# Optimization experiments

Measured on AMD Instinct MI355X. Metric: run time of the kernel, lower is better.

## Reference

```python
import jax, jax.numpy as jnp
import numpy as np

B, T, E = 4, 2048, 512
H, D = 8, 64            # num_heads, head_size = E // H
HID = H * E             # FFN hidden = num_heads * n_embed (per source)
EPS = 1e-5


def layer_norm(x, g, b):
    mu = jnp.mean(x, axis=-1, keepdims=True)
    var = jnp.var(x, axis=-1, keepdims=True)
    return (x - mu) * jax.lax.rsqrt(var + EPS) * g + b


def setup_inputs() -> dict:
    key = jax.random.key(0)
    ks = jax.random.split(key, 12)
    s_e = 1.0 / np.sqrt(E)
    s_hd = 1.0 / np.sqrt(H * D)
    s_hid = 1.0 / np.sqrt(HID)
    return {
        "x": jax.random.normal(ks[0], (B, T, E), jnp.float32),
        "Wq": jax.random.normal(ks[1], (H, E, D), jnp.float32) * s_e,
        "Wk": jax.random.normal(ks[2], (H, E, D), jnp.float32) * s_e,
        "Wv": jax.random.normal(ks[3], (H, E, D), jnp.float32) * s_e,
        "Wo": jax.random.normal(ks[4], (H * D, E), jnp.float32) * s_hd,
        "bo": jnp.zeros((E,), jnp.float32),
        "W1": jax.random.normal(ks[5], (E, HID), jnp.float32) * s_e,
        "b1": jnp.zeros((HID,), jnp.float32),
        "W2": jax.random.normal(ks[6], (HID, E), jnp.float32) * s_hid,
        "b2": jnp.zeros((E,), jnp.float32),
        "g1": jnp.ones((E,), jnp.float32),
        "be1": jnp.zeros((E,), jnp.float32),
        "g2": jnp.ones((E,), jnp.float32),
        "be2": jnp.zeros((E,), jnp.float32),
    }


def reference(x, Wq, Wk, Wv, Wo, bo, W1, b1, W2, b2, g1, be1, g2, be2):
    # pre-LN decoder block (layer_norm_first=True path)
    xn = layer_norm(x, g1, be1)

    # multi-head causal attention; NOTE: scale is T**-0.5 per the source code
    q = jnp.einsum('bte,hed->bhtd', xn, Wq)
    k = jnp.einsum('bte,hed->bhtd', xn, Wk)
    v = jnp.einsum('bte,hed->bhtd', xn, Wv)
    scores = jnp.einsum('bhtd,bhsd->bhts', q, k) * (T ** -0.5)
    causal = jnp.tril(jnp.ones((T, T), bool))
    scores = jnp.where(causal, scores, -jnp.inf)
    attn = jax.nn.softmax(scores, axis=-1)
    o = jnp.einsum('bhts,bhsd->bhtd', attn, v)           # [B,H,T,D]
    o = o.transpose(0, 2, 1, 3).reshape(B, T, H * D)      # concat heads
    mha = o @ Wo + bo

    x = xn + mha
    xn2 = layer_norm(x, g2, be2)
    ffn = jax.nn.relu(xn2 @ W1 + b1) @ W2 + b2
    return xn2 + ffn
```

## Files before the change

kernel.cpp:

```cpp
#include <hip/hip_runtime.h>
#include <hip/hip_bf16.h>
#include <math.h>

#define Bsz 4
#define Tt 2048
#define Ee 512
#define Hh 8
#define Dd 64
#define HIDs 4096
#define Mrows (Bsz * Tt)

typedef __attribute__((ext_vector_type(8))) short short8;
typedef __attribute__((ext_vector_type(4))) float f32x4;

#define AS1 __attribute__((address_space(1)))
#define AS3 __attribute__((address_space(3)))

__device__ __forceinline__ unsigned short f2bfu(float f) {
    unsigned u = __float_as_uint(f);
    return (unsigned short)((u + 0x7fffu + ((u >> 16) & 1u)) >> 16);
}
__device__ __forceinline__ unsigned short truncbf(float f) {
    return (unsigned short)(__float_as_uint(f) >> 16);
}
__device__ __forceinline__ unsigned scale2(unsigned w, float s) {
    float lo = __uint_as_float(w << 16) * s;
    float hi = __uint_as_float(w & 0xffff0000u) * s;
    return (unsigned)f2bfu(lo) | ((unsigned)f2bfu(hi) << 16);
}

__global__ __launch_bounds__(256) void ln_kernel(const float* __restrict__ x,
        const float* __restrict__ g, const float* __restrict__ b,
        const float* __restrict__ addb,
        float* __restrict__ out_f, __hip_bfloat16* __restrict__ out_bf) {
    int row = blockIdx.x;
    int tid = threadIdx.x;
    const float* xr = x + (size_t)row * Ee;
    float v0 = xr[tid];
    float v1 = xr[tid + 256];
    float s = v0 + v1;
    float sq = v0 * v0 + v1 * v1;
#pragma unroll
    for (int off = 32; off > 0; off >>= 1) {
        s  += __shfl_xor(s, off, 64);
        sq += __shfl_xor(sq, off, 64);
    }
    __shared__ float ls[4], lq[4];
    int wid = tid >> 6, lane = tid & 63;
    if (lane == 0) { ls[wid] = s; lq[wid] = sq; }
    __syncthreads();
    s  = ls[0] + ls[1] + ls[2] + ls[3];
    sq = lq[0] + lq[1] + lq[2] + lq[3];
    float mean = s * (1.0f / Ee);
    float var  = sq * (1.0f / Ee) - mean * mean;
    float rstd = rsqrtf(var + 1e-5f);
    float o0 = (v0 - mean) * rstd * g[tid]       + b[tid];
    float o1 = (v1 - mean) * rstd * g[tid + 256] + b[tid + 256];
    float* orow = out_f + (size_t)row * Ee;
    orow[tid]       = o0 + addb[tid];
    orow[tid + 256] = o1 + addb[tid + 256];
    __hip_bfloat16* brow = out_bf + (size_t)row * Ee;
    brow[tid]       = __float2bfloat16(o0);
    brow[tid + 256] = __float2bfloat16(o1);
}

__device__ __forceinline__ void tr_tile(const float* __restrict__ in,
        __hip_bfloat16* __restrict__ outp, int R, int C, int c0, int r0) {
    __shared__ float tile[64][65];
    int tc = threadIdx.x & 63, tg = threadIdx.x >> 6;
#pragma unroll
    for (int i = 0; i < 16; ++i) {
        int r = tg * 16 + i;
        tile[r][tc] = in[(size_t)(r0 + r) * C + c0 + tc];
    }
    __syncthreads();
#pragma unroll
    for (int i = 0; i < 16; ++i) {
        int cc = tg * 16 + i;
        outp[(size_t)(c0 + cc) * R + r0 + tc] = __float2bfloat16(tile[tc][cc]);
    }
}
__global__ __launch_bounds__(256) void repack_all(const float* __restrict__ Wq,
        const float* __restrict__ Wk, const float* __restrict__ Wv,
        const float* __restrict__ Wo, const float* __restrict__ W1,
        const float* __restrict__ W2, __hip_bfloat16* __restrict__ bqT,
        __hip_bfloat16* __restrict__ woT, __hip_bfloat16* __restrict__ w1T,
        __hip_bfloat16* __restrict__ w2T) {
    int blk = blockIdx.x;
    if (blk < 192) {
        int p = blk >> 6, h = (blk >> 3) & 7, et = blk & 7;
        const float* W = (p == 0) ? Wq : ((p == 1) ? Wk : Wv);
        __shared__ float tile[64][65];
        int td = threadIdx.x & 63, tg = threadIdx.x >> 6;
#pragma unroll
        for (int i = 0; i < 16; ++i) {
            int e = tg * 16 + i;
            tile[e][td] = W[((size_t)h * Ee + et * 64 + e) * Dd + td];
        }
        __syncthreads();
#pragma unroll
        for (int i = 0; i < 16; ++i) {
            int d = tg * 16 + i;
            bqT[((size_t)(p * 512 + h * 64 + d)) * Ee + et * 64 + td] =
                __float2bfloat16(tile[td][d]);
        }
    } else if (blk < 256) {
        int t = blk - 192;
        tr_tile(Wo, woT, 512, 512, (t & 7) * 64, (t >> 3) * 64);
    } else if (blk < 768) {
        int t = blk - 256;
        tr_tile(W1, w1T, 512, HIDs, (t & 63) * 64, (t >> 6) * 64);
    } else {
        int t = blk - 768;
        tr_tile(W2, w2T, HIDs, 512, (t & 7) * 64, (t >> 3) * 64);
    }
}

__global__ __launch_bounds__(256) void mfma_gemm(
        const __hip_bfloat16* __restrict__ A, int lda,
        const __hip_bfloat16* __restrict__ B, int ldb,
        __hip_bfloat16* __restrict__ Cb, int ldc, int K, int nx) {
    __shared__ __hip_bfloat16 As[2 * 128 * 32];
    __shared__ __hip_bfloat16 Bs[2 * 128 * 32];
    int tid = threadIdx.x;
    int lane = tid & 63, wave = tid >> 6;
    int wm = wave >> 1, wn = wave & 1;
    int L = blockIdx.x;
    int slots = (int)gridDim.x >> 3;
    int v = (L & 7) * slots + (L >> 3);
    int bx = v % nx, by = v / nx;
    int row0 = by * 128, col0 = bx * 128;
    f32x4 acc[4][4];
#pragma unroll
    for (int i = 0; i < 4; ++i)
#pragma unroll
        for (int j = 0; j < 4; ++j) acc[i][j] = (f32x4){0.f, 0.f, 0.f, 0.f};

    int fr = lane & 15;
    int kq = (lane >> 4) << 3;

    for (int k0 = 0; k0 < K; k0 += 64) {
        __syncthreads();
#pragma unroll
        for (int j = 0; j < 4; ++j) {
            int c  = j * 256 + tid;
            int cb = j * 256 + wave * 64;
            int p  = c >> 9, cp = c & 511;
            int r  = cp >> 2, kg = (cp & 3) << 3;
            int ko = k0 + p * 32 + kg;
            __builtin_amdgcn_global_load_lds(
                (const AS1 void*)(A + (size_t)(row0 + r) * lda + ko),
                (AS3 void*)(As + cb * 8), 16, 0, 0);
            __builtin_amdgcn_global_load_lds(
                (const AS1 void*)(B + (size_t)(col0 + r) * ldb + ko),
                (AS3 void*)(Bs + cb * 8), 16, 0, 0);
        }
        __syncthreads();
#pragma unroll
        for (int ks = 0; ks < 2; ++ks) {
            short8 afr[4], bfr[4];
#pragma unroll
            for (int i = 0; i < 4; ++i) {
                afr[i] = *(const short8*)(As + ks * 4096 + (wm * 64 + i * 16 + fr) * 32 + kq);
                bfr[i] = *(const short8*)(Bs + ks * 4096 + (wn * 64 + i * 16 + fr) * 32 + kq);
            }
#pragma unroll
            for (int i = 0; i < 4; ++i)
#pragma unroll
                for (int j = 0; j < 4; ++j)
                    acc[i][j] = __builtin_amdgcn_mfma_f32_16x16x32_bf16(afr[i], bfr[j], acc[i][j], 0, 0, 0);
        }
    }
    int rq = (lane >> 4) << 2;
#pragma unroll
    for (int i = 0; i < 4; ++i)
#pragma unroll
        for (int j = 0; j < 4; ++j)
#pragma unroll
            for (int gidx = 0; gidx < 4; ++gidx) {
                int r = row0 + wm * 64 + i * 16 + rq + gidx;
                int c = col0 + wn * 64 + j * 16 + fr;
                Cb[(size_t)r * ldc + c] = __float2bfloat16(acc[i][j][gidx]);
            }
}

__global__ __launch_bounds__(256) void mfma_gemm_n64(
        const __hip_bfloat16* __restrict__ A, int lda,
        const __hip_bfloat16* __restrict__ B, int ldb,
        float* __restrict__ Cf, int ldc, int K, int nx) {
    __shared__ __hip_bfloat16 As[2 * 128 * 32];
    __shared__ __hip_bfloat16 Bs[2 * 64 * 32];
    int tid = threadIdx.x;
    int lane = tid & 63, wave = tid >> 6;
    int L = blockIdx.x;
    int slots = (int)gridDim.x >> 3;
    int v = (L & 7) * slots + (L >> 3);
    int bx = v % nx, by = v / nx;
    int row0 = by * 128, col0 = bx * 64;
    f32x4 acc[2][4];
#pragma unroll
    for (int i = 0; i < 2; ++i)
#pragma unroll
        for (int j = 0; j < 4; ++j) acc[i][j] = (f32x4){0.f, 0.f, 0.f, 0.f};

    int fr = lane & 15;
    int kq = (lane >> 4) << 3;

    for (int k0 = 0; k0 < K; k0 += 64) {
        __syncthreads();
#pragma unroll
        for (int j = 0; j < 4; ++j) {
            int c  = j * 256 + tid;
            int cb = j * 256 + wave * 64;
            int p  = c >> 9, cp = c & 511;
            int r  = cp >> 2, kg = (cp & 3) << 3;
            __builtin_amdgcn_global_load_lds(
                (const AS1 void*)(A + (size_t)(row0 + r) * lda + k0 + p * 32 + kg),
                (AS3 void*)(As + cb * 8), 16, 0, 0);
        }
#pragma unroll
        for (int j = 0; j < 2; ++j) {
            int c  = j * 256 + tid;
            int cb = j * 256 + wave * 64;
            int p  = c >> 8, cp = c & 255;
            int r  = cp >> 2, kg = (cp & 3) << 3;
            __builtin_amdgcn_global_load_lds(
                (const AS1 void*)(B + (size_t)(col0 + r) * ldb + k0 + p * 32 + kg),
                (AS3 void*)(Bs + cb * 8), 16, 0, 0);
        }
        __syncthreads();
#pragma unroll
        for (int ks = 0; ks < 2; ++ks) {
            short8 afr[2], bfr[4];
#pragma unroll
            for (int i = 0; i < 2; ++i)
                afr[i] = *(const short8*)(As + ks * 4096 + (wave * 32 + i * 16 + fr) * 32 + kq);
#pragma unroll
            for (int j = 0; j < 4; ++j)
                bfr[j] = *(const short8*)(Bs + ks * 2048 + (j * 16 + fr) * 32 + kq);
#pragma unroll
            for (int i = 0; i < 2; ++i)
#pragma unroll
                for (int j = 0; j < 4; ++j)
                    acc[i][j] = __builtin_amdgcn_mfma_f32_16x16x32_bf16(afr[i], bfr[j], acc[i][j], 0, 0, 0);
        }
    }
    int rq = (lane >> 4) << 2;
#pragma unroll
    for (int i = 0; i < 2; ++i)
#pragma unroll
        for (int j = 0; j < 4; ++j)
#pragma unroll
            for (int gidx = 0; gidx < 4; ++gidx) {
                int r = row0 + wave * 32 + i * 16 + rq + gidx;
                int c = col0 + j * 16 + fr;
                Cf[(size_t)r * ldc + c] += acc[i][j][gidx];
            }
}

__global__ __launch_bounds__(256) void mfma_gemm256(
        const __hip_bfloat16* __restrict__ A, int lda,
        const __hip_bfloat16* __restrict__ B, int ldb,
        __hip_bfloat16* __restrict__ Cb, int ldc, int K,
        const float* __restrict__ bias) {
    __shared__ __hip_bfloat16 As[2 * 256 * 32];
    __shared__ __hip_bfloat16 Bs[2 * 128 * 32];
    int tid = threadIdx.x;
    int lane = tid & 63, wave = tid >> 6;
    int L = blockIdx.x;
    int k8 = L & 7, sub = L >> 3;
    int sr = k8 >> 1, sc = k8 & 1;
    int by = sr * 8 + (sub >> 4);
    int bx = sc * 16 + (sub & 15);
    int row0 = by * 256, col0 = bx * 128;
    f32x4 acc[4][8];
#pragma unroll
    for (int i = 0; i < 4; ++i)
#pragma unroll
        for (int j = 0; j < 8; ++j) acc[i][j] = (f32x4){0.f, 0.f, 0.f, 0.f};

    int fr = lane & 15;
    int kq = (lane >> 4) << 3;

    for (int k0 = 0; k0 < K; k0 += 64) {
        __syncthreads();
#pragma unroll
        for (int j = 0; j < 8; ++j) {
            int c  = j * 256 + tid;
            int cb = j * 256 + wave * 64;
            int p  = c >> 10, cp = c & 1023;
            int r  = cp >> 2, kg = (cp & 3) << 3;
            __builtin_amdgcn_global_load_lds(
                (const AS1 void*)(A + (size_t)(row0 + r) * lda + k0 + p * 32 + kg),
                (AS3 void*)(As + cb * 8), 16, 0, 0);
        }
#pragma unroll
        for (int j = 0; j < 4; ++j) {
            int c  = j * 256 + tid;
            int cb = j * 256 + wave * 64;
            int p  = c >> 9, cp = c & 511;
            int r  = cp >> 2, kg = (cp & 3) << 3;
            __builtin_amdgcn_global_load_lds(
                (const AS1 void*)(B + (size_t)(col0 + r) * ldb + k0 + p * 32 + kg),
                (AS3 void*)(Bs + cb * 8), 16, 0, 0);
        }
        __syncthreads();
#pragma unroll
        for (int ks = 0; ks < 2; ++ks) {
            short8 afr[4], bfr[8];
#pragma unroll
            for (int i = 0; i < 4; ++i)
                afr[i] = *(const short8*)(As + ks * 8192 + (wave * 64 + i * 16 + fr) * 32 + kq);
#pragma unroll
            for (int j = 0; j < 8; ++j)
                bfr[j] = *(const short8*)(Bs + ks * 4096 + (j * 16 + fr) * 32 + kq);
#pragma unroll
            for (int i = 0; i < 4; ++i)
#pragma unroll
                for (int j = 0; j < 8; ++j)
                    acc[i][j] = __builtin_amdgcn_mfma_f32_16x16x32_bf16(afr[i], bfr[j], acc[i][j], 0, 0, 0);
        }
    }
    int rq = (lane >> 4) << 2;
    float bv[8];
#pragma unroll
    for (int j = 0; j < 8; ++j) bv[j] = bias[col0 + j * 16 + fr];
#pragma unroll
    for (int i = 0; i < 4; ++i)
#pragma unroll
        for (int j = 0; j < 8; ++j)
#pragma unroll
            for (int gidx = 0; gidx < 4; ++gidx) {
                int r = row0 + wave * 64 + i * 16 + rq + gidx;
                int c = col0 + j * 16 + fr;
                float t = acc[i][j][gidx] + bv[j];
                Cb[(size_t)r * ldc + c] = __float2bfloat16(t > 0.f ? t : 0.f);
            }
}

__global__ __launch_bounds__(512) void attn_mfma(const __hip_bfloat16* __restrict__ qkvb,
        __hip_bfloat16* __restrict__ ob) {
    __shared__ __hip_bfloat16 KsS[64 * 72];
    __shared__ __hip_bfloat16 VtS[64 * 72];
    __shared__ __hip_bfloat16 PsS[8 * 16 * 72];
    __hip_bfloat16* Qs = PsS;

    const unsigned short* q16 = (const unsigned short*)qkvb;
    int tid  = threadIdx.x;
    int lane = tid & 63, wave = tid >> 6;
    int g = lane >> 4, c = lane & 15;
    int blk = blockIdx.x;
    int qb  = 15 - (blk >> 5);
    int bh  = blk & 31;
    int b = bh >> 3, h = bh & 7;
    int base = qb * 128;
    size_t tokbase = (size_t)b * Tt;
    int qoff = h * 64, koff = 512 + h * 64, voff = 1024 + h * 64;
    const float qscale = 0.022097086912079608f * 1.4426950408889634f;

    {
        int q = tid >> 2, dg = (tid & 3) * 16;
        const unsigned short* src = q16 + (tokbase + base + q) * 1536 + qoff + dg;
        uint4 a  = *(const uint4*)src;
        uint4 b4 = *(const uint4*)(src + 8);
        uint4 ra, rb;
        ra.x = scale2(a.x, qscale);  ra.y = scale2(a.y, qscale);
        ra.z = scale2(a.z, qscale);  ra.w = scale2(a.w, qscale);
        rb.x = scale2(b4.x, qscale); rb.y = scale2(b4.y, qscale);
        rb.z = scale2(b4.z, qscale); rb.w = scale2(b4.w, qscale);
        *(uint4*)(Qs + q * 72 + dg)     = ra;
        *(uint4*)(Qs + q * 72 + dg + 8) = rb;
    }
    __syncthreads();
    short8 aq[2];
    aq[0] = *(const short8*)(Qs + (wave * 16 + c) * 72 + g * 8);
    aq[1] = *(const short8*)(Qs + (wave * 16 + c) * 72 + 32 + g * 8);

    short8 ones;
#pragma unroll
    for (int i = 0; i < 8; ++i) ones[i] = (short)0x3F80;

    f32x4 acc[4];
#pragma unroll
    for (int dt = 0; dt < 4; ++dt) acc[dt] = (f32x4){0.f, 0.f, 0.f, 0.f};
    f32x4 accL = (f32x4){0.f, 0.f, 0.f, 0.f};
    __hip_bfloat16* Psw = PsS + wave * (16 * 72);
    unsigned short* Psw16 = (unsigned short*)Psw;

    int tmax = 2 * qb + 1;
    for (int tile = 0; tile <= tmax; ++tile) {
        int s0 = tile * 64;
        __syncthreads();
        {
            int s = tid >> 3, dg = (tid & 7) * 8;
            *(uint4*)(KsS + s * 72 + dg) =
                *(const uint4*)(q16 + (tokbase + s0 + s) * 1536 + koff + dg);
        }
        {
            int sp = (tid & 31) * 2, dg4 = (tid >> 5) * 4;
            const unsigned short* r0p = q16 + (tokbase + s0 + sp) * 1536 + voff + dg4;
            uint2 va = *(const uint2*)r0p;
            uint2 vb = *(const uint2*)(r0p + 1536);
            unsigned a0[2] = {va.x, va.y};
            unsigned b0[2] = {vb.x, vb.y};
#pragma unroll
            for (int i = 0; i < 2; ++i) {
                unsigned p0 = (a0[i] & 0xffffu) | (b0[i] << 16);
                unsigned p1 = (a0[i] >> 16) | (b0[i] & 0xffff0000u);
                *(unsigned*)(VtS + (dg4 + 2 * i) * 72 + sp)     = p0;
                *(unsigned*)(VtS + (dg4 + 2 * i + 1) * 72 + sp) = p1;
            }
        }
        __syncthreads();
        if (tile == tmax && wave < 4) continue;
        f32x4 Sc[4];
#pragma unroll
        for (int st = 0; st < 4; ++st) Sc[st] = (f32x4){0.f, 0.f, 0.f, 0.f};
#pragma unroll
        for (int ks = 0; ks < 2; ++ks)
#pragma unroll
            for (int st = 0; st < 4; ++st) {
                short8 bk = *(const short8*)(KsS + (st * 16 + c) * 72 + ks * 32 + g * 8);
                Sc[st] = __builtin_amdgcn_mfma_f32_16x16x32_bf16(aq[ks], bk, Sc[st], 0, 0, 0);
            }
        if (tile >= 2 * qb) {
            int qg = base + wave * 16 + g * 4;
#pragma unroll
            for (int st = 0; st < 4; ++st) {
                int sg = s0 + st * 16 + c;
#pragma unroll
                for (int r = 0; r < 4; ++r)
                    if (sg > qg + r) Sc[st][r] = -1e30f;
            }
        }
#pragma unroll
        for (int st = 0; st < 4; ++st)
#pragma unroll
            for (int r = 0; r < 4; ++r)
                Psw16[(g * 4 + r) * 72 + st * 16 + c] =
                    truncbf(__builtin_amdgcn_exp2f(Sc[st][r]));
#pragma unroll
        for (int ks = 0; ks < 2; ++ks) {
            short8 ap = *(const short8*)(Psw + c * 72 + ks * 32 + g * 8);
            accL = __builtin_amdgcn_mfma_f32_16x16x32_bf16(ap, ones, accL, 0, 0, 0);
#pragma unroll
            for (int dt = 0; dt < 4; ++dt) {
                short8 bv = *(const short8*)(VtS + (dt * 16 + c) * 72 + ks * 32 + g * 8);
                acc[dt] = __builtin_amdgcn_mfma_f32_16x16x32_bf16(ap, bv, acc[dt], 0, 0, 0);
            }
        }
    }
    float rl[4];
#pragma unroll
    for (int r = 0; r < 4; ++r) rl[r] = 1.0f / accL[r];
#pragma unroll
    for (int dt = 0; dt < 4; ++dt)
#pragma unroll
        for (int r = 0; r < 4; ++r) {
            int row = base + wave * 16 + g * 4 + r;
            float o = acc[dt][r] * rl[r];
            ob[(tokbase + row) * 512 + h * 64 + dt * 16 + c] = __float2bfloat16(o);
        }
}

extern "C" void kernel_launch(void* const* d_in, const int* in_sizes, int n_in,
                              void* d_out, int out_size, void* d_ws, size_t ws_size,
                              hipStream_t stream) {
    const float* x   = (const float*)d_in[0];
    const float* Wq  = (const float*)d_in[1];
    const float* Wk  = (const float*)d_in[2];
    const float* Wv  = (const float*)d_in[3];
    const float* Wo  = (const float*)d_in[4];
    const float* bo  = (const float*)d_in[5];
    const float* W1  = (const float*)d_in[6];
    const float* b1  = (const float*)d_in[7];
    const float* W2  = (const float*)d_in[8];
    const float* b2  = (const float*)d_in[9];
    const float* g1  = (const float*)d_in[10];
    const float* be1 = (const float*)d_in[11];
    const float* g2  = (const float*)d_in[12];
    const float* be2 = (const float*)d_in[13];
    float* out = (float*)d_out;

    char* ws = (char*)d_ws;
    __hip_bfloat16* bqT    = (__hip_bfloat16*)(ws);
    __hip_bfloat16* woT    = (__hip_bfloat16*)(ws + 1572864);
    __hip_bfloat16* w1T    = (__hip_bfloat16*)(ws + 2097152);
    __hip_bfloat16* w2T    = (__hip_bfloat16*)(ws + 6291456);
    float*          xn     = (float*)(ws + 10485760);
    __hip_bfloat16* xn_bf  = (__hip_bfloat16*)(ws + 27262976);
    __hip_bfloat16* qkv_bf = (__hip_bfloat16*)(ws + 35651584);
    __hip_bfloat16* o_bf   = (__hip_bfloat16*)(ws + 60817408);
    __hip_bfloat16* h_bf   = (__hip_bfloat16*)(ws + 35651584);

    ln_kernel<<<Mrows, 256, 0, stream>>>(x, g1, be1, bo, xn, xn_bf);
    repack_all<<<1280, 256, 0, stream>>>(Wq, Wk, Wv, Wo, W1, W2, bqT, woT, w1T, w2T);
    mfma_gemm<<<768, 256, 0, stream>>>(
        xn_bf, 512, bqT, 512, qkv_bf, 1536, 512, 12);
    attn_mfma<<<Bsz * Hh * (Tt / 128), 512, 0, stream>>>(qkv_bf, o_bf);
    mfma_gemm_n64<<<512, 256, 0, stream>>>(
        o_bf, 512, woT, 512, xn, 512, 512, 8);
    ln_kernel<<<Mrows, 256, 0, stream>>>(xn, g2, be2, b2, out, xn_bf);
    mfma_gemm256<<<1024, 256, 0, stream>>>(
        xn_bf, 512, w1T, 512, h_bf, HIDs, 512, b1);
    mfma_gemm_n64<<<512, 256, 0, stream>>>(
        h_bf, HIDs, w2T, HIDs, out, 512, HIDs, 8);
}
```

Measured before the change: 355.2 us.

## Fold Q scale into weights, double-buffer GEMM, prefetch K/V in attention

The softmax scale and log2e factor move into the Wq repack, so the attention kernel no longer rescales Q tiles at load. The FFN-style GEMM drops from a 64-wide K step with two syncs to a 32-wide double-buffered LDS pipeline that issues the next stage's loads before the current MFMAs. The attention kernel prefetches the next K/V tile into registers while computing on the current one. Together these aim to hide global-load latency and remove per-tile ALU work. The cost is more register pressure, and Q is now rounded to bf16 once after scaling instead of being rescaled in the kernel.

Measured after the change: 342.3 us. -3.6%, faster.

```diff
diff --git a/kernel.cpp b/kernel.cpp
--- a/kernel.cpp
+++ b/kernel.cpp
@@ -22,11 +22,6 @@
 }
 __device__ __forceinline__ unsigned short truncbf(float f) {
     return (unsigned short)(__float_as_uint(f) >> 16);
-}
-__device__ __forceinline__ unsigned scale2(unsigned w, float s) {
-    float lo = __uint_as_float(w << 16) * s;
-    float hi = __uint_as_float(w & 0xffff0000u) * s;
-    return (unsigned)f2bfu(lo) | ((unsigned)f2bfu(hi) << 16);
 }
 
 __global__ __launch_bounds__(256) void ln_kernel(const float* __restrict__ x,
@@ -90,12 +85,13 @@
     if (blk < 192) {
         int p = blk >> 6, h = (blk >> 3) & 7, et = blk & 7;
         const float* W = (p == 0) ? Wq : ((p == 1) ? Wk : Wv);
+        float sc = (p == 0) ? 0.022097086912079608f * 1.4426950408889634f : 1.0f;
         __shared__ float tile[64][65];
         int td = threadIdx.x & 63, tg = threadIdx.x >> 6;
 #pragma unroll
         for (int i = 0; i < 16; ++i) {
             int e = tg * 16 + i;
-            tile[e][td] = W[((size_t)h * Ee + et * 64 + e) * Dd + td];
+            tile[e][td] = W[((size_t)h * Ee + et * 64 + e) * Dd + td] * sc;
         }
         __syncthreads();
 #pragma unroll
@@ -281,46 +277,52 @@
 
     int fr = lane & 15;
     int kq = (lane >> 4) << 3;
-
-    for (int k0 = 0; k0 < K; k0 += 64) {
-        __syncthreads();
-#pragma unroll
-        for (int j = 0; j < 8; ++j) {
-            int c  = j * 256 + tid;
-            int cb = j * 256 + wave * 64;
-            int p  = c >> 10, cp = c & 1023;
-            int r  = cp >> 2, kg = (cp & 3) << 3;
-            __builtin_amdgcn_global_load_lds(
-                (const AS1 void*)(A + (size_t)(row0 + r) * lda + k0 + p * 32 + kg),
-                (AS3 void*)(As + cb * 8), 16, 0, 0);
-        }
-#pragma unroll
-        for (int j = 0; j < 4; ++j) {
-            int c  = j * 256 + tid;
-            int cb = j * 256 + wave * 64;
-            int p  = c >> 9, cp = c & 511;
-            int r  = cp >> 2, kg = (cp & 3) << 3;
-            __builtin_amdgcn_global_load_lds(
-                (const AS1 void*)(B + (size_t)(col0 + r) * ldb + k0 + p * 32 + kg),
-                (AS3 void*)(Bs + cb * 8), 16, 0, 0);
-        }
-        __syncthreads();
-#pragma unroll
-        for (int ks = 0; ks < 2; ++ks) {
-            short8 afr[4], bfr[8];
-#pragma unroll
-            for (int i = 0; i < 4; ++i)
-                afr[i] = *(const short8*)(As + ks * 8192 + (wave * 64 + i * 16 + fr) * 32 + kq);
+    int nsteps = K >> 5;
+
+#define STAGE256(st, buf)                                                     \
+    do {                                                                      \
+        int ko_ = (st) << 5;                                                  \
+        _Pragma("unroll")                                                     \
+        for (int j = 0; j < 4; ++j) {                                         \
+            int c = j * 256 + tid;                                            \
+            int cb = j * 256 + wave * 64;                                     \
+            int r = c >> 2, kg = (c & 3) << 3;                                \
+            __builtin_amdgcn_global_load_lds(                                 \
+                (const AS1 void*)(A + (size_t)(row0 + r) * lda + ko_ + kg),   \
+                (AS3 void*)(As + (buf) * 8192 + cb * 8), 16, 0, 0);           \
+        }                                                                     \
+        _Pragma("unroll")                                                     \
+        for (int j = 0; j < 2; ++j) {                                         \
+            int c = j * 256 + tid;                                            \
+            int cb = j * 256 + wave * 64;                                     \
+            int r = c >> 2, kg = (c & 3) << 3;                                \
+            __builtin_amdgcn_global_load_lds(                                 \
+                (const AS1 void*)(B + (size_t)(col0 + r) * ldb + ko_ + kg),   \
+                (AS3 void*)(Bs + (buf) * 4096 + cb * 8), 16, 0, 0);           \
+        }                                                                     \
+    } while (0)
+
+    STAGE256(0, 0);
+    __syncthreads();
+    for (int st = 0; st < nsteps; ++st) {
+        int buf = st & 1;
+        if (st + 1 < nsteps) STAGE256(st + 1, buf ^ 1);
+        short8 afr[4], bfr[8];
+#pragma unroll
+        for (int i = 0; i < 4; ++i)
+            afr[i] = *(const short8*)(As + buf * 8192 + (wave * 64 + i * 16 + fr) * 32 + kq);
+#pragma unroll
+        for (int j = 0; j < 8; ++j)
+            bfr[j] = *(const short8*)(Bs + buf * 4096 + (j * 16 + fr) * 32 + kq);
+#pragma unroll
+        for (int i = 0; i < 4; ++i)
 #pragma unroll
             for (int j = 0; j < 8; ++j)
-                bfr[j] = *(const short8*)(Bs + ks * 4096 + (j * 16 + fr) * 32 + kq);
-#pragma unroll
-            for (int i = 0; i < 4; ++i)
-#pragma unroll
-                for (int j = 0; j < 8; ++j)
-                    acc[i][j] = __builtin_amdgcn_mfma_f32_16x16x32_bf16(afr[i], bfr[j], acc[i][j], 0, 0, 0);
-        }
-    }
+                acc[i][j] = __builtin_amdgcn_mfma_f32_16x16x32_bf16(afr[i], bfr[j], acc[i][j], 0, 0, 0);
+        __syncthreads();
+    }
+#undef STAGE256
+
     int rq = (lane >> 4) << 2;
     float bv[8];
 #pragma unroll
@@ -356,20 +358,14 @@
     int base = qb * 128;
     size_t tokbase = (size_t)b * Tt;
     int qoff = h * 64, koff = 512 + h * 64, voff = 1024 + h * 64;
-    const float qscale = 0.022097086912079608f * 1.4426950408889634f;
 
     {
         int q = tid >> 2, dg = (tid & 3) * 16;
         const unsigned short* src = q16 + (tokbase + base + q) * 1536 + qoff + dg;
         uint4 a  = *(const uint4*)src;
         uint4 b4 = *(const uint4*)(src + 8);
-        uint4 ra, rb;
-        ra.x = scale2(a.x, qscale);  ra.y = scale2(a.y, qscale);
-        ra.z = scale2(a.z, qscale);  ra.w = scale2(a.w, qscale);
-        rb.x = scale2(b4.x, qscale); rb.y = scale2(b4.y, qscale);
-        rb.z = scale2(b4.z, qscale); rb.w = scale2(b4.w, qscale);
-        *(uint4*)(Qs + q * 72 + dg)     = ra;
-        *(uint4*)(Qs + q * 72 + dg + 8) = rb;
+        *(uint4*)(Qs + q * 72 + dg)     = a;
+        *(uint4*)(Qs + q * 72 + dg + 8) = b4;
     }
     __syncthreads();
     short8 aq[2];
@@ -387,20 +383,21 @@
     __hip_bfloat16* Psw = PsS + wave * (16 * 72);
     unsigned short* Psw16 = (unsigned short*)Psw;
 
+    int s_k = tid >> 3, dg_k = (tid & 7) * 8;
+    int sp = (tid & 31) * 2, dg4 = (tid >> 5) * 4;
+    uint4 kreg; uint2 va, vb;
+    {
+        kreg = *(const uint4*)(q16 + (tokbase + s_k) * 1536 + koff + dg_k);
+        const unsigned short* r0p = q16 + (tokbase + sp) * 1536 + voff + dg4;
+        va = *(const uint2*)r0p;
+        vb = *(const uint2*)(r0p + 1536);
+    }
+
     int tmax = 2 * qb + 1;
     for (int tile = 0; tile <= tmax; ++tile) {
-        int s0 = tile * 64;
-        __syncthreads();
+        __syncthreads();
+        *(uint4*)(KsS + s_k * 72 + dg_k) = kreg;
         {
-            int s = tid >> 3, dg = (tid & 7) * 8;
-            *(uint4*)(KsS + s * 72 + dg) =
-                *(const uint4*)(q16 + (tokbase + s0 + s) * 1536 + koff + dg);
-        }
-        {
-            int sp = (tid & 31) * 2, dg4 = (tid >> 5) * 4;
-            const unsigned short* r0p = q16 + (tokbase + s0 + sp) * 1536 + voff + dg4;
-            uint2 va = *(const uint2*)r0p;
-            uint2 vb = *(const uint2*)(r0p + 1536);
             unsigned a0[2] = {va.x, va.y};
             unsigned b0[2] = {vb.x, vb.y};
 #pragma unroll
@@ -412,6 +409,13 @@
             }
         }
         __syncthreads();
+        if (tile < tmax) {
+            int s1 = (tile + 1) * 64;
+            kreg = *(const uint4*)(q16 + (tokbase + s1 + s_k) * 1536 + koff + dg_k);
+            const unsigned short* r0p = q16 + (tokbase + s1 + sp) * 1536 + voff + dg4;
+            va = *(const uint2*)r0p;
+            vb = *(const uint2*)(r0p + 1536);
+        }
         if (tile == tmax && wave < 4) continue;
         f32x4 Sc[4];
 #pragma unroll
@@ -424,6 +428,7 @@
                 Sc[st] = __builtin_amdgcn_mfma_f32_16x16x32_bf16(aq[ks], bk, Sc[st], 0, 0, 0);
             }
         if (tile >= 2 * qb) {
+            int s0 = tile * 64;
             int qg = base + wave * 16 + g * 4;
 #pragma unroll
             for (int st = 0; st < 4; ++st) {
```
